# Optimization experiments

Hardware: AMD Instinct MI355X
Metric: run time of the kernel (lower is better)

Reference implementation:

```python
import jax, jax.numpy as jnp
import numpy as np

M = 0.4        # margin
H = 0.333      # margin scaler slope
S = 64.0       # logit scale
BN_MEAN = 20.0     # running_mean of norm normalizer (affine=False, eval stats)
BN_VAR = 100.0 * 100.0
BN_EPS = 1e-3


def setup_inputs() -> dict:
    key = jax.random.key(0)
    k1, k2, k3 = jax.random.split(key, 3)
    embs = jax.random.normal(k1, (1024, 512), dtype=jnp.float32)
    weight = jax.random.normal(k2, (100000, 512), dtype=jnp.float32)
    labels = jax.random.randint(k3, (1024,), 0, 100000)
    return {"embs": embs, "weight": weight, "labels": labels}


def reference(embs, weight, labels):
    n = embs.shape[0]
    rows = jnp.arange(n)
    # feature norms and cosine logits
    norms = jnp.linalg.norm(embs, axis=1, keepdims=True)            # [N,1]
    w_norm = weight / jnp.linalg.norm(weight, axis=1, keepdims=True)  # [C,D]
    logits = (embs / norms) @ w_norm.T                               # [N,C]
    # norm-adaptive margin scaler (BatchNorm1d with running stats, affine=False)
    g = (norms[:, 0] - BN_MEAN) / jnp.sqrt(BN_VAR + BN_EPS)
    g = jnp.clip(g * H, -1.0, 1.0)                                   # [N]
    # angular margin at the label position
    theta = jnp.arccos(jnp.clip(logits.astype(jnp.float32), -0.999, 0.999))
    theta = theta.at[rows, labels].add(-M * g)
    logits_m = jnp.cos(jnp.clip(theta, 0.0, jnp.pi))
    # additive margin at the label position
    logits_m = logits_m.at[rows, labels].add(-(1.0 + M) * g)
    # scaled softmax cross-entropy (mean over batch)
    logp = jax.nn.log_softmax(logits_m * S, axis=-1)
    return -jnp.mean(logp[rows, labels])
```

## Files before the change

kernel.cpp:

```cpp
#include <hip/hip_runtime.h>
#include <math.h>

constexpr int N_ROWS = 1024;
constexpr int DDIM   = 512;
constexpr int C_CLS  = 100000;
constexpr float MARG = 0.4f;
constexpr int NT8    = 784;
constexpr int WPAD8  = 100352;
constexpr int NT_FB  = 782;

typedef __attribute__((ext_vector_type(8))) short bf16x8;
typedef __attribute__((ext_vector_type(4))) float f32x4;
typedef __attribute__((ext_vector_type(4))) int   i32x4;
typedef __attribute__((ext_vector_type(8))) int   i32x8;
typedef __attribute__((address_space(1))) const void gvoid_t;
typedef __attribute__((address_space(3))) void lvoid_t;

#define WAITV(N) asm volatile("s_waitcnt vmcnt(" #N ")" ::: "memory")

__device__ __forceinline__ unsigned int f2bf(float x) {
    union { float f; unsigned int u; } v; v.f = x;
    return (v.u + 0x7FFFu + ((v.u >> 16) & 1u)) >> 16;
}

__device__ __forceinline__ float wave_sum(float s) {
    #pragma unroll
    for (int m = 1; m < 64; m <<= 1) s += __shfl_xor(s, m, 64);
    return s;
}

#if __has_builtin(__builtin_amdgcn_cvt_pk_fp8_f32)
__device__ __forceinline__ unsigned int pk4_e4m3(float a, float b, float c, float d) {
    unsigned int u = (unsigned int)__builtin_amdgcn_cvt_pk_fp8_f32(a, b, 0, false);
    u = (unsigned int)__builtin_amdgcn_cvt_pk_fp8_f32(c, d, (int)u, true);
    return u;
}
#else
__device__ __forceinline__ unsigned int sw_e4m3(float x) {
    x = fminf(fmaxf(x, -448.f), 448.f);
    unsigned int s = (x < 0.f) ? 0x80u : 0u;
    float ax = fabsf(x);
    if (ax < 7.8125e-3f) {
        int q = (int)rintf(ax * 512.f);
        if (q >= 8) return s | 0x08;
        return s | (unsigned int)q;
    }
    int e; float m = frexpf(ax, &e);
    int q = (int)rintf(m * 16.f);
    if (q == 16) { q = 8; e += 1; }
    int E = e - 1 + 7;
    if (E > 15) { E = 15; q = 14; }
    return s | ((unsigned int)E << 3) | (unsigned int)(q - 8);
}
__device__ __forceinline__ unsigned int pk4_e4m3(float a, float b, float c, float d) {
    return sw_e4m3(a) | (sw_e4m3(b) << 8) | (sw_e4m3(c) << 16) | (sw_e4m3(d) << 24);
}
#endif

__global__ __launch_bounds__(256) void prep_embs8(const float* __restrict__ embs,
                                                  float* __restrict__ g,
                                                  unsigned char* __restrict__ ehat8) {
    const int row  = blockIdx.x * 4 + (threadIdx.x >> 6);
    const int lane = threadIdx.x & 63;
    const float4* src = (const float4*)(embs + (size_t)row * DDIM + lane * 8);
    const float4 a = src[0], b = src[1];
    float ss = a.x*a.x + a.y*a.y + a.z*a.z + a.w*a.w
             + b.x*b.x + b.y*b.y + b.z*b.z + b.w*b.w;
    ss = wave_sum(ss);
    const float norm = sqrtf(ss);
    const float rn = 1.f / norm;
    if (lane == 0) {
        float gg = (norm - 20.f) / sqrtf(10000.f + 1e-3f) * 0.333f;
        gg = fminf(fmaxf(gg, -1.f), 1.f);
        g[row] = gg;
    }
    uint2 pk;
    pk.x = pk4_e4m3(a.x*rn, a.y*rn, a.z*rn, a.w*rn);
    pk.y = pk4_e4m3(b.x*rn, b.y*rn, b.z*rn, b.w*rn);
    *(uint2*)(ehat8 + (size_t)row * DDIM + lane * 8) = pk;
}

__global__ __launch_bounds__(256) void prep_what8(const float* __restrict__ w,
                                                  unsigned char* __restrict__ what8) {
    const int row  = blockIdx.x * 4 + (threadIdx.x >> 6);
    const int lane = threadIdx.x & 63;
    const float4* src = (const float4*)(w + (size_t)row * DDIM + lane * 8);
    const float4 a = src[0], b = src[1];
    float ss = a.x*a.x + a.y*a.y + a.z*a.z + a.w*a.w
             + b.x*b.x + b.y*b.y + b.z*b.z + b.w*b.w;
    ss = wave_sum(ss);
    const float rn = rsqrtf(ss);
    uint2 pk;
    pk.x = pk4_e4m3(a.x*rn, a.y*rn, a.z*rn, a.w*rn);
    pk.y = pk4_e4m3(b.x*rn, b.y*rn, b.z*rn, b.w*rn);
    *(uint2*)(what8 + (size_t)row * DDIM + lane * 8) = pk;
}

__device__ __forceinline__ void stage8(const unsigned char* __restrict__ src, int grow0,
                                       unsigned char* tile, int kbase, int wv, int lane) {
    const int lr = lane >> 3;
    const int lc = (lane & 7) ^ lr;
    #pragma unroll
    for (int i = 0; i < 4; ++i) {
        const int s = wv * 4 + i;
        const unsigned char* gp = src + (size_t)(grow0 + s * 8 + lr) * DDIM + kbase + lc * 16;
        __builtin_amdgcn_global_load_lds((gvoid_t*)gp, (lvoid_t*)(tile + s * 1024), 16, 0, 0);
    }
}
__device__ __forceinline__ i32x8 frag8(const unsigned char* tile, int row, int lane) {
    const int c0 = ((lane >> 4) * 2 + 0) ^ (row & 7);
    const int c1 = ((lane >> 4) * 2 + 1) ^ (row & 7);
    const i32x4 lo = *(const i32x4*)(tile + row * 128 + c0 * 16);
    const i32x4 hi = *(const i32x4*)(tile + row * 128 + c1 * 16);
    i32x8 r;
    r[0] = lo[0]; r[1] = lo[1]; r[2] = lo[2]; r[3] = lo[3];
    r[4] = hi[0]; r[5] = hi[1]; r[6] = hi[2]; r[7] = hi[3];
    return r;
}

__global__ __launch_bounds__(256, 2) void gemm128f8(
        const unsigned char* __restrict__ ehat8,
        const unsigned char* __restrict__ what8,
        const int* __restrict__ labels,
        float* __restrict__ psum,
        float* __restrict__ dlab)
{
    __shared__ __align__(16) unsigned char Ab[2][128 * 128];
    __shared__ __align__(16) unsigned char Bb[2][128 * 128];
    __shared__ float redbuf[2][128];

    const int tid  = threadIdx.x;
    const int lane = tid & 63;
    const int wv   = tid >> 6;
    const int wr   = wv >> 1;
    const int wc   = wv & 1;

    const int wgid   = ((int)blockIdx.x & 7) * 784 + ((int)blockIdx.x >> 3);
    const int tile_c = wgid >> 3;
    const int tile_r = wgid & 7;
    const int row0   = tile_r * 128;
    const int col0   = tile_c * 128;

    f32x4 acc[4][4];
    #pragma unroll
    for (int m = 0; m < 4; ++m)
        #pragma unroll
        for (int n = 0; n < 4; ++n) acc[m][n] = f32x4{0.f, 0.f, 0.f, 0.f};

    stage8(ehat8, row0, Ab[0], 0,   wv, lane);
    stage8(what8, col0, Bb[0], 0,   wv, lane);
    stage8(ehat8, row0, Ab[1], 128, wv, lane);
    stage8(what8, col0, Bb[1], 128, wv, lane);
    WAITV(8);
    __builtin_amdgcn_s_barrier();

    #pragma unroll
    for (int t = 0; t < 4; ++t) {
        const unsigned char* At = Ab[t & 1];
        const unsigned char* Bt = Bb[t & 1];
        i32x8 aF[4], bF[4];
        #pragma unroll
        for (int m = 0; m < 4; ++m)
            aF[m] = frag8(At, wr * 64 + m * 16 + (lane & 15), lane);
        #pragma unroll
        for (int n = 0; n < 4; ++n)
            bF[n] = frag8(Bt, wc * 64 + n * 16 + (lane & 15), lane);
        asm volatile("s_waitcnt lgkmcnt(0)" ::: "memory");
        __builtin_amdgcn_sched_barrier(0);
        __builtin_amdgcn_s_barrier();
        if (t < 2) {
            stage8(ehat8, row0, Ab[t & 1], (t + 2) * 128, wv, lane);
            stage8(what8, col0, Bb[t & 1], (t + 2) * 128, wv, lane);
        }
        __builtin_amdgcn_s_setprio(1);
        #pragma unroll
        for (int m = 0; m < 4; ++m)
            #pragma unroll
            for (int n = 0; n < 4; ++n)
                acc[m][n] = __builtin_amdgcn_mfma_scale_f32_16x16x128_f8f6f4(
                                aF[m], bF[n], acc[m][n], 0, 0, 0, 127, 0, 127);
        __builtin_amdgcn_s_setprio(0);
        if (t < 2)      { WAITV(8); }
        else if (t == 2){ WAITV(0); }
        if (t < 3) __builtin_amdgcn_s_barrier();
    }

    #pragma unroll
    for (int m = 0; m < 4; ++m) {
        #pragma unroll
        for (int j = 0; j < 4; ++j) {
            const int lrow  = wr * 64 + m * 16 + ((lane >> 4) << 2) + j;
            const int r_abs = row0 + lrow;
            const int lab   = labels[r_abs];
            float s = 0.f;
            #pragma unroll
            for (int n = 0; n < 4; ++n) {
                const int c_abs = col0 + wc * 64 + n * 16 + (lane & 15);
                float v = acc[m][n][j];
                v = fminf(fmaxf(v, -0.999f), 0.999f);
                if (c_abs == lab) dlab[r_abs] = v;
                if (c_abs < C_CLS) s += __expf(64.f * v - 64.f);
            }
            #pragma unroll
            for (int msk = 1; msk < 16; msk <<= 1) s += __shfl_xor(s, msk, 64);
            if ((lane & 15) == 0) redbuf[wc][lrow] = s;
        }
    }
    __syncthreads();
    for (int t = tid; t < 128; t += 256)
        psum[(size_t)(row0 + t) * NT8 + tile_c] = redbuf[0][t] + redbuf[1][t];
}

__global__ __launch_bounds__(256) void prep_embs(const float* __restrict__ embs,
                                                 float* __restrict__ g,
                                                 unsigned short* __restrict__ ehat) {
    const int row  = blockIdx.x * 4 + (threadIdx.x >> 6);
    const int lane = threadIdx.x & 63;
    const float4* src = (const float4*)(embs + (size_t)row * DDIM + lane * 8);
    const float4 a = src[0], b = src[1];
    float ss = a.x*a.x + a.y*a.y + a.z*a.z + a.w*a.w
             + b.x*b.x + b.y*b.y + b.z*b.z + b.w*b.w;
    ss = wave_sum(ss);
    const float norm = sqrtf(ss);
    const float rn = 1.f / norm;
    if (lane == 0) {
        float gg = (norm - 20.f) / sqrtf(10000.f + 1e-3f) * 0.333f;
        gg = fminf(fmaxf(gg, -1.f), 1.f);
        g[row] = gg;
    }
    uint4 pk;
    pk.x = f2bf(a.x*rn) | (f2bf(a.y*rn) << 16);
    pk.y = f2bf(a.z*rn) | (f2bf(a.w*rn) << 16);
    pk.z = f2bf(b.x*rn) | (f2bf(b.y*rn) << 16);
    pk.w = f2bf(b.z*rn) | (f2bf(b.w*rn) << 16);
    *(uint4*)(ehat + (size_t)row * DDIM + lane * 8) = pk;
}

__global__ __launch_bounds__(256) void prep_wnorm(const float* __restrict__ w,
                                                  float* __restrict__ rnormw) {
    const int row  = blockIdx.x * 4 + (threadIdx.x >> 6);
    const int lane = threadIdx.x & 63;
    const float4* src = (const float4*)(w + (size_t)row * DDIM + lane * 8);
    const float4 a = src[0], b = src[1];
    float ss = a.x*a.x + a.y*a.y + a.z*a.z + a.w*a.w
             + b.x*b.x + b.y*b.y + b.z*b.z + b.w*b.w;
    ss = wave_sum(ss);
    if (lane == 0) rnormw[row] = 1.f / sqrtf(ss);
}

__global__ __launch_bounds__(256, 2) void gemm_fused_fb(
        const unsigned short* __restrict__ ehat,
        const float* __restrict__ weight,
        const float* __restrict__ rnormw,
        const int* __restrict__ labels,
        float* __restrict__ psum,
        float* __restrict__ dlab)
{
    constexpr int BM = 128, BN = 128, BK = 32;
    __shared__ __align__(16) unsigned short Asf[BM * BK];
    __shared__ __align__(16) unsigned short Bsf[BN * BK];
    __shared__ float redbuf[2][BM];

    const int bid    = blockIdx.x;
    const int tile_c = bid >> 3;
    const int tile_r = bid & 7;
    const int row0   = tile_r * BM;
    const int col0   = tile_c * BN;

    const int tid  = threadIdx.x;
    const int lane = tid & 63;
    const int wv   = tid >> 6;
    const int wr   = wv >> 1;
    const int wc   = wv & 1;

    f32x4 acc[4][4];
    #pragma unroll
    for (int m = 0; m < 4; ++m)
        #pragma unroll
        for (int n = 0; n < 4; ++n) acc[m][n] = f32x4{0.f, 0.f, 0.f, 0.f};

    const int kq    = tid & 7;
    const int brow0 = tid >> 3;
    int   cidx[4];
    float rnv[4];
    #pragma unroll
    for (int p = 0; p < 4; ++p) {
        int c = col0 + p * 32 + brow0;
        c = c < C_CLS ? c : C_CLS - 1;
        cidx[p] = c;
        rnv[p]  = rnormw[c];
    }

    for (int kt = 0; kt < DDIM / BK; ++kt) {
        const int kbase = kt * BK;
        #pragma unroll
        for (int call = 0; call < 2; ++call) {
            const int chunk = call * 256 + tid;
            const uint4 d = *(const uint4*)(ehat + (size_t)(row0 + (chunk >> 2)) * DDIM
                                            + kbase + (chunk & 3) * 8);
            *(uint4*)(Asf + chunk * 8) = d;
        }
        #pragma unroll
        for (int p = 0; p < 4; ++p) {
            const float4 wd = *(const float4*)(weight + (size_t)cidx[p] * DDIM + kbase + kq * 4);
            const float r = rnv[p];
            const unsigned int lo = f2bf(wd.x * r) | (f2bf(wd.y * r) << 16);
            const unsigned int hi = f2bf(wd.z * r) | (f2bf(wd.w * r) << 16);
            *(uint2*)(Bsf + (p * 32 + brow0) * BK + kq * 4) = make_uint2(lo, hi);
        }
        __syncthreads();
        bf16x8 af[4], bfr[4];
        const int lr  = lane & 15;
        const int lko = (lane >> 4) * 8;
        #pragma unroll
        for (int m = 0; m < 4; ++m)
            af[m] = *(const bf16x8*)(Asf + (wr * 64 + m * 16 + lr) * BK + lko);
        #pragma unroll
        for (int n = 0; n < 4; ++n)
            bfr[n] = *(const bf16x8*)(Bsf + (wc * 64 + n * 16 + lr) * BK + lko);
        #pragma unroll
        for (int m = 0; m < 4; ++m)
            #pragma unroll
            for (int n = 0; n < 4; ++n)
                acc[m][n] = __builtin_amdgcn_mfma_f32_16x16x32_bf16(af[m], bfr[n], acc[m][n], 0, 0, 0);
        __syncthreads();
    }

    #pragma unroll
    for (int m = 0; m < 4; ++m) {
        #pragma unroll
        for (int j = 0; j < 4; ++j) {
            const int lrow  = wr * 64 + m * 16 + ((lane >> 4) << 2) + j;
            const int r_abs = row0 + lrow;
            const int lab   = labels[r_abs];
            float s = 0.f;
            #pragma unroll
            for (int n = 0; n < 4; ++n) {
                const int c_abs = col0 + wc * 64 + n * 16 + (lane & 15);
                float v = acc[m][n][j];
                v = fminf(fmaxf(v, -0.999f), 0.999f);
                if (c_abs == lab) dlab[r_abs] = v;
                if (c_abs < C_CLS) s += __expf(64.f * v - 64.f);
            }
            #pragma unroll
            for (int msk = 1; msk < 16; msk <<= 1) s += __shfl_xor(s, msk, 64);
            if ((lane & 15) == 0) redbuf[wc][lrow] = s;
        }
    }
    __syncthreads();
    for (int t = tid; t < BM; t += 256)
        psum[(size_t)(row0 + t) * NT_FB + tile_c] = redbuf[0][t] + redbuf[1][t];
}

__global__ __launch_bounds__(256) void reduce_rows(const float* __restrict__ psum,
                                                   const float* __restrict__ dlab,
                                                   const float* __restrict__ g,
                                                   float* __restrict__ losses, int nt) {
    const int row  = blockIdx.x * 4 + (threadIdx.x >> 6);
    const int lane = threadIdx.x & 63;
    const float* p = psum + (size_t)row * nt;
    float s = 0.f;
    for (int t = lane; t < nt; t += 64) s += p[t];
    s = wave_sum(s);
    if (lane == 0) {
        const float v  = dlab[row];
        const float gg = g[row];
        float th = acosf(v) - MARG * gg;
        th = fminf(fmaxf(th, 0.f), 3.14159265358979323846f);
        const float vm = cosf(th) - (1.f + MARG) * gg;
        s = s - __expf(64.f * v - 64.f) + __expf(64.f * vm - 64.f);
        losses[row] = 64.f + logf(s) - 64.f * vm;
    }
}

__global__ __launch_bounds__(256) void final_mean(const float* __restrict__ losses,
                                                  float* __restrict__ out) {
    const int tid = threadIdx.x;
    float s = 0.f;
    #pragma unroll
    for (int i = 0; i < 4; ++i) s += losses[tid + i * 256];
    s = wave_sum(s);
    __shared__ float red[4];
    if ((tid & 63) == 0) red[tid >> 6] = s;
    __syncthreads();
    if (tid == 0) out[0] = (red[0] + red[1] + red[2] + red[3]) * (1.f / 1024.f);
}

extern "C" void kernel_launch(void* const* d_in, const int* in_sizes, int n_in,
                              void* d_out, int out_size, void* d_ws, size_t ws_size,
                              hipStream_t stream) {
    const float* embs   = (const float*)d_in[0];
    const float* weight = (const float*)d_in[1];
    const int*   labels = (const int*)d_in[2];
    float* out = (float*)d_out;
    unsigned char* wsb = (unsigned char*)d_ws;

    const size_t WHAT8_B = (size_t)WPAD8 * DDIM;
    const size_t EHAT8_B = (size_t)N_ROWS * DDIM;
    const size_t PSUM_B  = (size_t)N_ROWS * NT8 * 4;
    const size_t NEED_B  = WHAT8_B + EHAT8_B + PSUM_B + 3 * 4096;

    if (ws_size >= NEED_B) {
        unsigned char* what8 = wsb;
        unsigned char* ehat8 = wsb + WHAT8_B;
        float* psum   = (float*)(wsb + WHAT8_B + EHAT8_B);
        float* gbuf   = psum + (size_t)N_ROWS * NT8;
        float* dlab   = gbuf + 1024;
        float* losses = dlab + 1024;

        prep_embs8<<<N_ROWS / 4, 256, 0, stream>>>(embs, gbuf, ehat8);
        prep_what8<<<C_CLS / 4, 256, 0, stream>>>(weight, what8);
        gemm128f8<<<NT8 * 8, 256, 0, stream>>>(ehat8, what8, labels, psum, dlab);
        reduce_rows<<<N_ROWS / 4, 256, 0, stream>>>(psum, dlab, gbuf, losses, NT8);
        final_mean<<<1, 256, 0, stream>>>(losses, out);
    } else {
        float* ws = (float*)d_ws;
        float* rnormw = ws + 0;
        float* gbuf   = ws + 100352;
        float* dlab   = ws + 101376;
        float* losses = ws + 102400;
        unsigned short* ehat = (unsigned short*)(ws + 103424);
        float* psum   = ws + 103424 + 262144;

        prep_embs <<<N_ROWS / 4, 256, 0, stream>>>(embs, gbuf, ehat);
        prep_wnorm<<<C_CLS / 4, 256, 0, stream>>>(weight, rnormw);
        gemm_fused_fb<<<NT_FB * 8, 256, 0, stream>>>(ehat, weight, rnormw, labels, psum, dlab);
        reduce_rows<<<N_ROWS / 4, 256, 0, stream>>>(psum, dlab, gbuf, losses, NT_FB);
        final_mean<<<1, 256, 0, stream>>>(losses, out);
    }
}
```

Before: 178.7 us.

## Replace LDS-staged FP8 GEMM with direct-register loads and bf16 partial sums

```diff
diff --git a/kernel.cpp b/kernel.cpp
--- a/kernel.cpp
+++ b/kernel.cpp
@@ -5,7 +5,7 @@
 constexpr int DDIM   = 512;
 constexpr int C_CLS  = 100000;
 constexpr float MARG = 0.4f;
-constexpr int NT8    = 784;
+constexpr int NT64   = 1568;
 constexpr int WPAD8  = 100352;
 constexpr int NT_FB  = 782;
 
@@ -13,10 +13,6 @@
 typedef __attribute__((ext_vector_type(4))) float f32x4;
 typedef __attribute__((ext_vector_type(4))) int   i32x4;
 typedef __attribute__((ext_vector_type(8))) int   i32x8;
-typedef __attribute__((address_space(1))) const void gvoid_t;
-typedef __attribute__((address_space(3))) void lvoid_t;
-
-#define WAITV(N) asm volatile("s_waitcnt vmcnt(" #N ")" ::: "memory")
 
 __device__ __forceinline__ unsigned int f2bf(float x) {
     union { float f; unsigned int u; } v; v.f = x;
@@ -56,6 +52,17 @@
     return sw_e4m3(a) | (sw_e4m3(b) << 8) | (sw_e4m3(c) << 16) | (sw_e4m3(d) << 24);
 }
 #endif
+
+__device__ __forceinline__ float dec_e4m3(unsigned int b) {
+    const unsigned int E = (b >> 3) & 15u, M = b & 7u;
+    if (E) {
+        union { unsigned int u; float f; } v;
+        v.u = ((b & 0x80u) << 24) | ((E + 120u) << 23) | (M << 20);
+        return v.f;
+    }
+    float d = (float)M * 0.001953125f;
+    return (b & 0x80u) ? -d : d;
+}
 
 __global__ __launch_bounds__(256) void prep_embs8(const float* __restrict__ embs,
                                                   float* __restrict__ g,
@@ -84,6 +91,10 @@
                                                   unsigned char* __restrict__ what8) {
     const int row  = blockIdx.x * 4 + (threadIdx.x >> 6);
     const int lane = threadIdx.x & 63;
+    if (row >= C_CLS) {
+        *(uint2*)(what8 + (size_t)row * DDIM + lane * 8) = make_uint2(0u, 0u);
+        return;
+    }
     const float4* src = (const float4*)(w + (size_t)row * DDIM + lane * 8);
     const float4 a = src[0], b = src[1];
     float ss = a.x*a.x + a.y*a.y + a.z*a.z + a.w*a.w
@@ -96,38 +107,193 @@
     *(uint2*)(what8 + (size_t)row * DDIM + lane * 8) = pk;
 }
 
-__device__ __forceinline__ void stage8(const unsigned char* __restrict__ src, int grow0,
-                                       unsigned char* tile, int kbase, int wv, int lane) {
-    const int lr = lane >> 3;
-    const int lc = (lane & 7) ^ lr;
-    #pragma unroll
-    for (int i = 0; i < 4; ++i) {
-        const int s = wv * 4 + i;
-        const unsigned char* gp = src + (size_t)(grow0 + s * 8 + lr) * DDIM + kbase + lc * 16;
-        __builtin_amdgcn_global_load_lds((gvoid_t*)gp, (lvoid_t*)(tile + s * 1024), 16, 0, 0);
-    }
-}
-__device__ __forceinline__ i32x8 frag8(const unsigned char* tile, int row, int lane) {
-    const int c0 = ((lane >> 4) * 2 + 0) ^ (row & 7);
-    const int c1 = ((lane >> 4) * 2 + 1) ^ (row & 7);
-    const i32x4 lo = *(const i32x4*)(tile + row * 128 + c0 * 16);
-    const i32x4 hi = *(const i32x4*)(tile + row * 128 + c1 * 16);
-    i32x8 r;
-    r[0] = lo[0]; r[1] = lo[1]; r[2] = lo[2]; r[3] = lo[3];
-    r[4] = hi[0]; r[5] = hi[1]; r[6] = hi[2]; r[7] = hi[3];
-    return r;
-}
-
-__global__ __launch_bounds__(256, 2) void gemm128f8(
+__device__ __forceinline__ i32x8 join8(i32x4 lo, i32x4 hi) {
+    return __builtin_shufflevector(lo, hi, 0, 1, 2, 3, 4, 5, 6, 7);
+}
+
+__global__ __launch_bounds__(256, 2) void gemm_direct(
         const unsigned char* __restrict__ ehat8,
         const unsigned char* __restrict__ what8,
+        unsigned short* __restrict__ psum)
+{
+    const int tid  = threadIdx.x;
+    const int lane = tid & 63;
+    const int wv   = tid >> 6;
+
+    const int wgid   = ((int)blockIdx.x & 7) * 784 + ((int)blockIdx.x >> 3);
+    const int tile_c = wgid >> 2;
+    const int row0   = (wgid & 3) * 256 + wv * 64;
+    const int col0   = tile_c * 64;
+
+    const int q = lane >> 4;
+    const int r = lane & 15;
+
+    const unsigned char* abase = ehat8 + (size_t)(row0 + r) * DDIM + q * 32;
+    const unsigned char* bbase = what8 + (size_t)(col0 + r) * DDIM + q * 32;
+
+    f32x4 acc[4][4];
+    #pragma unroll
+    for (int m = 0; m < 4; ++m)
+        #pragma unroll
+        for (int n = 0; n < 4; ++n) acc[m][n] = f32x4{0.f, 0.f, 0.f, 0.f};
+
+    i32x4 a0[4][2], b0[4][2], a1[4][2], b1[4][2];
+
+#define LDT(A, B, T) do {                                                       \
+    _Pragma("unroll")                                                           \
+    for (int m = 0; m < 4; ++m) {                                               \
+        A[m][0] = *(const i32x4*)(abase + m * 16 * DDIM + (T) * 128);           \
+        A[m][1] = *(const i32x4*)(abase + m * 16 * DDIM + (T) * 128 + 16);      \
+    }                                                                           \
+    _Pragma("unroll")                                                           \
+    for (int n = 0; n < 4; ++n) {                                               \
+        B[n][0] = *(const i32x4*)(bbase + n * 16 * DDIM + (T) * 128);           \
+        B[n][1] = *(const i32x4*)(bbase + n * 16 * DDIM + (T) * 128 + 16);      \
+    }                                                                           \
+} while (0)
+
+#define MMT(A, B) do {                                                          \
+    __builtin_amdgcn_s_setprio(1);                                              \
+    _Pragma("unroll")                                                           \
+    for (int m = 0; m < 4; ++m)                                                 \
+        _Pragma("unroll")                                                       \
+        for (int n = 0; n < 4; ++n)                                             \
+            acc[m][n] = __builtin_amdgcn_mfma_scale_f32_16x16x128_f8f6f4(       \
+                join8(A[m][0], A[m][1]), join8(B[n][0], B[n][1]),               \
+                acc[m][n], 0, 0, 0, 127, 0, 127);                               \
+    __builtin_amdgcn_s_setprio(0);                                              \
+} while (0)
+
+    LDT(a0, b0, 0);
+    LDT(a1, b1, 1);
+    MMT(a0, b0);
+    __builtin_amdgcn_sched_barrier(0);
+    LDT(a0, b0, 2);
+    MMT(a1, b1);
+    __builtin_amdgcn_sched_barrier(0);
+    LDT(a1, b1, 3);
+    MMT(a0, b0);
+    __builtin_amdgcn_sched_barrier(0);
+    MMT(a1, b1);
+#undef LDT
+#undef MMT
+
+    #pragma unroll
+    for (int m = 0; m < 4; ++m) {
+        #pragma unroll
+        for (int j = 0; j < 4; ++j) {
+            float s = 0.f;
+            #pragma unroll
+            for (int n = 0; n < 4; ++n) {
+                float v = acc[m][n][j];
+                v = fminf(fmaxf(v, -0.999f), 0.999f);
+                s += __expf(64.f * v - 64.f);
+            }
+            s += __shfl_xor(s, 1, 64);
+            s += __shfl_xor(s, 2, 64);
+            s += __shfl_xor(s, 4, 64);
+            s += __shfl_xor(s, 8, 64);
+            if (r == 0) {
+                const int r_abs = row0 + m * 16 + q * 4 + j;
+                psum[(size_t)r_abs * NT64 + tile_c] = (unsigned short)f2bf(s);
+            }
+        }
+    }
+}
+
+__global__ __launch_bounds__(256) void reduce_rows8(
+        const unsigned short* __restrict__ psum,
+        const unsigned char* __restrict__ ehat8,
+        const unsigned char* __restrict__ what8,
+        const int* __restrict__ labels,
+        const float* __restrict__ g,
+        float* __restrict__ losses) {
+    const int row  = blockIdx.x * 4 + (threadIdx.x >> 6);
+    const int lane = threadIdx.x & 63;
+    const unsigned short* p = psum + (size_t)row * NT64;
+    float s = 0.f;
+    for (int t = lane; t < NT64; t += 64) {
+        union { unsigned int u; float f; } w; w.u = ((unsigned int)p[t]) << 16;
+        s += w.f;
+    }
+    const int lab = labels[row];
+    const uint2 ea = *(const uint2*)(ehat8 + (size_t)row * DDIM + lane * 8);
+    const uint2 wa = *(const uint2*)(what8 + (size_t)lab * DDIM + lane * 8);
+    float d = 0.f;
+    #pragma unroll
+    for (int i = 0; i < 4; ++i)
+        d += dec_e4m3((ea.x >> (8 * i)) & 0xFFu) * dec_e4m3((wa.x >> (8 * i)) & 0xFFu);
+    #pragma unroll
+    for (int i = 0; i < 4; ++i)
+        d += dec_e4m3((ea.y >> (8 * i)) & 0xFFu) * dec_e4m3((wa.y >> (8 * i)) & 0xFFu);
+    s = wave_sum(s);
+    d = wave_sum(d);
+    if (lane == 0) {
+        const float v  = fminf(fmaxf(d, -0.999f), 0.999f);
+        const float gg = g[row];
+        float th = acosf(v) - MARG * gg;
+        th = fminf(fmaxf(th, 0.f), 3.14159265358979323846f);
+        const float vm = cosf(th) - (1.f + MARG) * gg;
+        s = s - __expf(64.f * v - 64.f) + __expf(64.f * vm - 64.f);
+        losses[row] = 64.f + logf(s) - 64.f * vm;
+    }
+}
+
+__global__ __launch_bounds__(256) void prep_embs(const float* __restrict__ embs,
+                                                 float* __restrict__ g,
+                                                 unsigned short* __restrict__ ehat) {
+    const int row  = blockIdx.x * 4 + (threadIdx.x >> 6);
+    const int lane = threadIdx.x & 63;
+    const float4* src = (const float4*)(embs + (size_t)row * DDIM + lane * 8);
+    const float4 a = src[0], b = src[1];
+    float ss = a.x*a.x + a.y*a.y + a.z*a.z + a.w*a.w
+             + b.x*b.x + b.y*b.y + b.z*b.z + b.w*b.w;
+    ss = wave_sum(ss);
+    const float norm = sqrtf(ss);
+    const float rn = 1.f / norm;
+    if (lane == 0) {
+        float gg = (norm - 20.f) / sqrtf(10000.f + 1e-3f) * 0.333f;
+        gg = fminf(fmaxf(gg, -1.f), 1.f);
+        g[row] = gg;
+    }
+    uint4 pk;
+    pk.x = f2bf(a.x*rn) | (f2bf(a.y*rn) << 16);
+    pk.y = f2bf(a.z*rn) | (f2bf(a.w*rn) << 16);
+    pk.z = f2bf(b.x*rn) | (f2bf(b.y*rn) << 16);
+    pk.w = f2bf(b.z*rn) | (f2bf(b.w*rn) << 16);
+    *(uint4*)(ehat + (size_t)row * DDIM + lane * 8) = pk;
+}
+
+__global__ __launch_bounds__(256) void prep_wnorm(const float* __restrict__ w,
+                                                  float* __restrict__ rnormw) {
+    const int row  = blockIdx.x * 4 + (threadIdx.x >> 6);
+    const int lane = threadIdx.x & 63;
+    const float4* src = (const float4*)(w + (size_t)row * DDIM + lane * 8);
+    const float4 a = src[0], b = src[1];
+    float ss = a.x*a.x + a.y*a.y + a.z*a.z + a.w*a.w
+             + b.x*b.x + b.y*b.y + b.z*b.z + b.w*b.w;
+    ss = wave_sum(ss);
+    if (lane == 0) rnormw[row] = 1.f / sqrtf(ss);
+}
+
+__global__ __launch_bounds__(256, 2) void gemm_fused_fb(
+        const unsigned short* __restrict__ ehat,
+        const float* __restrict__ weight,
+        const float* __restrict__ rnormw,
         const int* __restrict__ labels,
         float* __restrict__ psum,
         float* __restrict__ dlab)
 {
-    __shared__ __align__(16) unsigned char Ab[2][128 * 128];
-    __shared__ __align__(16) unsigned char Bb[2][128 * 128];
-    __shared__ float redbuf[2][128];
+    constexpr int BM = 128, BN = 128, BK = 32;
+    __shared__ __align__(16) unsigned short Asf[BM * BK];
+    __shared__ __align__(16) unsigned short Bsf[BN * BK];
+    __shared__ float redbuf[2][BM];
+
+    const int bid    = blockIdx.x;
+    const int tile_c = bid >> 3;
+    const int tile_r = bid & 7;
+    const int row0   = tile_r * BM;
+    const int col0   = tile_c * BN;
 
     const int tid  = threadIdx.x;
     const int lane = tid & 63;
@@ -135,54 +301,57 @@
     const int wr   = wv >> 1;
     const int wc   = wv & 1;
 
-    const int wgid   = ((int)blockIdx.x & 7) * 784 + ((int)blockIdx.x >> 3);
-    const int tile_c = wgid >> 3;
-    const int tile_r = wgid & 7;
-    const int row0   = tile_r * 128;
-    const int col0   = tile_c * 128;
-
     f32x4 acc[4][4];
     #pragma unroll
     for (int m = 0; m < 4; ++m)
         #pragma unroll
         for (int n = 0; n < 4; ++n) acc[m][n] = f32x4{0.f, 0.f, 0.f, 0.f};
 
-    stage8(ehat8, row0, Ab[0], 0,   wv, lane);
-    stage8(what8, col0, Bb[0], 0,   wv, lane);
-    stage8(ehat8, row0, Ab[1], 128, wv, lane);
-    stage8(what8, col0, Bb[1], 128, wv, lane);
-    WAITV(8);
-    __builtin_amdgcn_s_barrier();
-
-    #pragma unroll
-    for (int t = 0; t < 4; ++t) {
-        const unsigned char* At = Ab[t & 1];
-        const unsigned char* Bt = Bb[t & 1];
-        i32x8 aF[4], bF[4];
+    const int kq    = tid & 7;
+    const int brow0 = tid >> 3;
+    int   cidx[4];
+    float rnv[4];
+    #pragma unroll
+    for (int p = 0; p < 4; ++p) {
+        int c = col0 + p * 32 + brow0;
+        c = c < C_CLS ? c : C_CLS - 1;
+        cidx[p] = c;
+        rnv[p]  = rnormw[c];
+    }
+
+    for (int kt = 0; kt < DDIM / BK; ++kt) {
+        const int kbase = kt * BK;
+        #pragma unroll
+        for (int call = 0; call < 2; ++call) {
+            const int chunk = call * 256 + tid;
+            const uint4 dd = *(const uint4*)(ehat + (size_t)(row0 + (chunk >> 2)) * DDIM
+                                             + kbase + (chunk & 3) * 8);
+            *(uint4*)(Asf + chunk * 8) = dd;
+        }
+        #pragma unroll
+        for (int p = 0; p < 4; ++p) {
+            const float4 wd = *(const float4*)(weight + (size_t)cidx[p] * DDIM + kbase + kq * 4);
+            const float rr = rnv[p];
+            const unsigned int lo = f2bf(wd.x * rr) | (f2bf(wd.y * rr) << 16);
+            const unsigned int hi = f2bf(wd.z * rr) | (f2bf(wd.w * rr) << 16);
+            *(uint2*)(Bsf + (p * 32 + brow0) * BK + kq * 4) = make_uint2(lo, hi);
+        }
+        __syncthreads();
+        bf16x8 af[4], bfr[4];
+        const int lr  = lane & 15;
+        const int lko = (lane >> 4) * 8;
         #pragma unroll
         for (int m = 0; m < 4; ++m)
-            aF[m] = frag8(At, wr * 64 + m * 16 + (lane & 15), lane);
+            af[m] = *(const bf16x8*)(Asf + (wr * 64 + m * 16 + lr) * BK + lko);
         #pragma unroll
         for (int n = 0; n < 4; ++n)
-            bF[n] = frag8(Bt, wc * 64 + n * 16 + (lane & 15), lane);
-        asm volatile("s_waitcnt lgkmcnt(0)" ::: "memory");
-        __builtin_amdgcn_sched_barrier(0);
-        __builtin_amdgcn_s_barrier();
-        if (t < 2) {
-            stage8(ehat8, row0, Ab[t & 1], (t + 2) * 128, wv, lane);
-            stage8(what8, col0, Bb[t & 1], (t + 2) * 128, wv, lane);
-        }
-        __builtin_amdgcn_s_setprio(1);
+            bfr[n] = *(const bf16x8*)(Bsf + (wc * 64 + n * 16 + lr) * BK + lko);
         #pragma unroll
         for (int m = 0; m < 4; ++m)
             #pragma unroll
             for (int n = 0; n < 4; ++n)
-                acc[m][n] = __builtin_amdgcn_mfma_scale_f32_16x16x128_f8f6f4(
-                                aF[m], bF[n], acc[m][n], 0, 0, 0, 127, 0, 127);
-        __builtin_amdgcn_s_setprio(0);
-        if (t < 2)      { WAITV(8); }
-        else if (t == 2){ WAITV(0); }
-        if (t < 3) __builtin_amdgcn_s_barrier();
+                acc[m][n] = __builtin_amdgcn_mfma_f32_16x16x32_bf16(af[m], bfr[n], acc[m][n], 0, 0, 0);
+        __syncthreads();
     }
 
     #pragma unroll
@@ -207,147 +376,6 @@
         }
     }
     __syncthreads();
-    for (int t = tid; t < 128; t += 256)
-        psum[(size_t)(row0 + t) * NT8 + tile_c] = redbuf[0][t] + redbuf[1][t];
-}
-
-__global__ __launch_bounds__(256) void prep_embs(const float* __restrict__ embs,
-                                                 float* __restrict__ g,
-                                                 unsigned short* __restrict__ ehat) {
-    const int row  = blockIdx.x * 4 + (threadIdx.x >> 6);
-    const int lane = threadIdx.x & 63;
-    const float4* src = (const float4*)(embs + (size_t)row * DDIM + lane * 8);
-    const float4 a = src[0], b = src[1];
-    float ss = a.x*a.x + a.y*a.y + a.z*a.z + a.w*a.w
-             + b.x*b.x + b.y*b.y + b.z*b.z + b.w*b.w;
-    ss = wave_sum(ss);
-    const float norm = sqrtf(ss);
-    const float rn = 1.f / norm;
-    if (lane == 0) {
-        float gg = (norm - 20.f) / sqrtf(10000.f + 1e-3f) * 0.333f;
-        gg = fminf(fmaxf(gg, -1.f), 1.f);
-        g[row] = gg;
-    }
-    uint4 pk;
-    pk.x = f2bf(a.x*rn) | (f2bf(a.y*rn) << 16);
-    pk.y = f2bf(a.z*rn) | (f2bf(a.w*rn) << 16);
-    pk.z = f2bf(b.x*rn) | (f2bf(b.y*rn) << 16);
-    pk.w = f2bf(b.z*rn) | (f2bf(b.w*rn) << 16);
-    *(uint4*)(ehat + (size_t)row * DDIM + lane * 8) = pk;
-}
-
-__global__ __launch_bounds__(256) void prep_wnorm(const float* __restrict__ w,
-                                                  float* __restrict__ rnormw) {
-    const int row  = blockIdx.x * 4 + (threadIdx.x >> 6);
-    const int lane = threadIdx.x & 63;
-    const float4* src = (const float4*)(w + (size_t)row * DDIM + lane * 8);
-    const float4 a = src[0], b = src[1];
-    float ss = a.x*a.x + a.y*a.y + a.z*a.z + a.w*a.w
-             + b.x*b.x + b.y*b.y + b.z*b.z + b.w*b.w;
-    ss = wave_sum(ss);
-    if (lane == 0) rnormw[row] = 1.f / sqrtf(ss);
-}
-
-__global__ __launch_bounds__(256, 2) void gemm_fused_fb(
-        const unsigned short* __restrict__ ehat,
-        const float* __restrict__ weight,
-        const float* __restrict__ rnormw,
-        const int* __restrict__ labels,
-        float* __restrict__ psum,
-        float* __restrict__ dlab)
-{
-    constexpr int BM = 128, BN = 128, BK = 32;
-    __shared__ __align__(16) unsigned short Asf[BM * BK];
-    __shared__ __align__(16) unsigned short Bsf[BN * BK];
-    __shared__ float redbuf[2][BM];
-
-    const int bid    = blockIdx.x;
-    const int tile_c = bid >> 3;
-    const int tile_r = bid & 7;
-    const int row0   = tile_r * BM;
-    const int col0   = tile_c * BN;
-
-    const int tid  = threadIdx.x;
-    const int lane = tid & 63;
-    const int wv   = tid >> 6;
-    const int wr   = wv >> 1;
-    const int wc   = wv & 1;
-
-    f32x4 acc[4][4];
-    #pragma unroll
-    for (int m = 0; m < 4; ++m)
-        #pragma unroll
-        for (int n = 0; n < 4; ++n) acc[m][n] = f32x4{0.f, 0.f, 0.f, 0.f};
-
-    const int kq    = tid & 7;
-    const int brow0 = tid >> 3;
-    int   cidx[4];
-    float rnv[4];
-    #pragma unroll
-    for (int p = 0; p < 4; ++p) {
-        int c = col0 + p * 32 + brow0;
-        c = c < C_CLS ? c : C_CLS - 1;
-        cidx[p] = c;
-        rnv[p]  = rnormw[c];
-    }
-
-    for (int kt = 0; kt < DDIM / BK; ++kt) {
-        const int kbase = kt * BK;
-        #pragma unroll
-        for (int call = 0; call < 2; ++call) {
-            const int chunk = call * 256 + tid;
-            const uint4 d = *(const uint4*)(ehat + (size_t)(row0 + (chunk >> 2)) * DDIM
-                                            + kbase + (chunk & 3) * 8);
-            *(uint4*)(Asf + chunk * 8) = d;
-        }
-        #pragma unroll
-        for (int p = 0; p < 4; ++p) {
-            const float4 wd = *(const float4*)(weight + (size_t)cidx[p] * DDIM + kbase + kq * 4);
-            const float r = rnv[p];
-            const unsigned int lo = f2bf(wd.x * r) | (f2bf(wd.y * r) << 16);
-            const unsigned int hi = f2bf(wd.z * r) | (f2bf(wd.w * r) << 16);
-            *(uint2*)(Bsf + (p * 32 + brow0) * BK + kq * 4) = make_uint2(lo, hi);
-        }
-        __syncthreads();
-        bf16x8 af[4], bfr[4];
-        const int lr  = lane & 15;
-        const int lko = (lane >> 4) * 8;
-        #pragma unroll
-        for (int m = 0; m < 4; ++m)
-            af[m] = *(const bf16x8*)(Asf + (wr * 64 + m * 16 + lr) * BK + lko);
-        #pragma unroll
-        for (int n = 0; n < 4; ++n)
-            bfr[n] = *(const bf16x8*)(Bsf + (wc * 64 + n * 16 + lr) * BK + lko);
-        #pragma unroll
-        for (int m = 0; m < 4; ++m)
-            #pragma unroll
-            for (int n = 0; n < 4; ++n)
-                acc[m][n] = __builtin_amdgcn_mfma_f32_16x16x32_bf16(af[m], bfr[n], acc[m][n], 0, 0, 0);
-        __syncthreads();
-    }
-
-    #pragma unroll
-    for (int m = 0; m < 4; ++m) {
-        #pragma unroll
-        for (int j = 0; j < 4; ++j) {
-            const int lrow  = wr * 64 + m * 16 + ((lane >> 4) << 2) + j;
-            const int r_abs = row0 + lrow;
-            const int lab   = labels[r_abs];
-            float s = 0.f;
-            #pragma unroll
-            for (int n = 0; n < 4; ++n) {
-                const int c_abs = col0 + wc * 64 + n * 16 + (lane & 15);
-                float v = acc[m][n][j];
-                v = fminf(fmaxf(v, -0.999f), 0.999f);
-                if (c_abs == lab) dlab[r_abs] = v;
-                if (c_abs < C_CLS) s += __expf(64.f * v - 64.f);
-            }
-            #pragma unroll
-            for (int msk = 1; msk < 16; msk <<= 1) s += __shfl_xor(s, msk, 64);
-            if ((lane & 15) == 0) redbuf[wc][lrow] = s;
-        }
-    }
-    __syncthreads();
     for (int t = tid; t < BM; t += 256)
         psum[(size_t)(row0 + t) * NT_FB + tile_c] = redbuf[0][t] + redbuf[1][t];
 }
@@ -397,21 +425,20 @@
 
     const size_t WHAT8_B = (size_t)WPAD8 * DDIM;
     const size_t EHAT8_B = (size_t)N_ROWS * DDIM;
-    const size_t PSUM_B  = (size_t)N_ROWS * NT8 * 4;
-    const size_t NEED_B  = WHAT8_B + EHAT8_B + PSUM_B + 3 * 4096;
+    const size_t PSUM_B  = (size_t)N_ROWS * NT64 * 2;
+    const size_t NEED_B  = WHAT8_B + EHAT8_B + PSUM_B + 2 * 4096;
 
     if (ws_size >= NEED_B) {
         unsigned char* what8 = wsb;
         unsigned char* ehat8 = wsb + WHAT8_B;
-        float* psum   = (float*)(wsb + WHAT8_B + EHAT8_B);
-        float* gbuf   = psum + (size_t)N_ROWS * NT8;
-        float* dlab   = gbuf + 1024;
-        float* losses = dlab + 1024;
+        unsigned short* psum = (unsigned short*)(wsb + WHAT8_B + EHAT8_B);
+        float* gbuf   = (float*)(wsb + WHAT8_B + EHAT8_B + PSUM_B);
+        float* losses = gbuf + 1024;
 
         prep_embs8<<<N_ROWS / 4, 256, 0, stream>>>(embs, gbuf, ehat8);
-        prep_what8<<<C_CLS / 4, 256, 0, stream>>>(weight, what8);
-        gemm128f8<<<NT8 * 8, 256, 0, stream>>>(ehat8, what8, labels, psum, dlab);
-        reduce_rows<<<N_ROWS / 4, 256, 0, stream>>>(psum, dlab, gbuf, losses, NT8);
+        prep_what8<<<WPAD8 / 4, 256, 0, stream>>>(weight, what8);
+        gemm_direct<<<NT64 * 4, 256, 0, stream>>>(ehat8, what8, psum);
+        reduce_rows8<<<N_ROWS / 4, 256, 0, stream>>>(psum, ehat8, what8, labels, gbuf, losses);
         final_mean<<<1, 256, 0, stream>>>(losses, out);
     } else {
         float* ws = (float*)d_ws;
```

Result: slower. 272.8 us (+52.6%).
